# Performance work log

Hardware: AMD Instinct MI355X
Metric: run time of the kernel (lower is better)

The kernel has to match this reference:

```python
import jax, jax.numpy as jnp
import numpy as np


def _gcn_layer(x, W, b, src, dst, norm, n_nodes):
    # PyG GCNConv: h = x @ W, then degree-normalized scatter-add over edges (incl. self loops), then + bias
    h = x @ W                                   # [N, F_out]
    msg = h[src] * norm[:, None]                # [E+N, F_out]
    out = jax.ops.segment_sum(msg, dst, num_segments=n_nodes)
    return out + b


def _norm_and_loops(edge_index, n_nodes):
    # add self loops, compute symmetric normalization deg^-1/2[src]*deg^-1/2[dst]
    loop = jnp.arange(n_nodes, dtype=edge_index.dtype)
    src = jnp.concatenate([edge_index[0], loop])
    dst = jnp.concatenate([edge_index[1], loop])
    deg = jax.ops.segment_sum(jnp.ones_like(dst, dtype=jnp.float32), dst, num_segments=n_nodes)
    dinv = jnp.where(deg > 0, jax.lax.rsqrt(deg), 0.0)
    norm = dinv[src] * dinv[dst]
    return src, dst, norm


def setup_inputs() -> dict:
    key = jax.random.key(0)
    k1, k2, k3, k4 = jax.random.split(key, 4)
    N, E, F = 100000, 1600000, 512
    x = jax.random.normal(k1, (N, F), dtype=jnp.float32)
    edge_index = jax.random.randint(k2, (2, E), 0, N, dtype=jnp.int64)
    W1 = jax.random.normal(k3, (F, 128), dtype=jnp.float32) * (1.0 / np.sqrt(F))
    b1 = jnp.zeros((128,), dtype=jnp.float32)
    W2 = jax.random.normal(k4, (128, 64), dtype=jnp.float32) * (1.0 / np.sqrt(128))
    b2 = jnp.zeros((64,), dtype=jnp.float32)
    return {"x": x, "edge_index": edge_index, "W1": W1, "b1": b1, "W2": W2, "b2": b2}


def reference(x, edge_index, W1, b1, W2, b2):
    n_nodes = x.shape[0]
    src, dst, norm = _norm_and_loops(edge_index, n_nodes)
    h = jax.nn.relu(_gcn_layer(x, W1, b1, src, dst, norm, n_nodes))
    z = jax.nn.relu(_gcn_layer(h, W2, b2, src, dst, norm, n_nodes))
    return z
```

## Files before the change

### kernel.cpp

```cpp
#include <hip/hip_runtime.h>

#define SCAN_B 1024

using f16x8 = __attribute__((ext_vector_type(8))) _Float16;
using f32x4 = __attribute__((ext_vector_type(4))) float;
typedef _Float16 half4v __attribute__((ext_vector_type(4)));
typedef _Float16 half8v __attribute__((ext_vector_type(8)));


__global__ void init_kernel(int* __restrict__ cnt, int* __restrict__ fillc, int N,
                            const float* __restrict__ W1, _Float16* __restrict__ W1t, int K1, int N1,
                            const float* __restrict__ W2, _Float16* __restrict__ W2t, int K2, int N2) {
  int i = blockIdx.x * blockDim.x + threadIdx.x;
  if (i < N) { cnt[i] = 0; fillc[i] = 0; }
  const int n1 = K1 * N1;
  if (i < n1) {
    int k = i / N1, n = i % N1;
    W1t[(size_t)n * K1 + k] = (_Float16)W1[i];
  } else if (i < n1 + K2 * N2) {
    int j = i - n1;
    int k = j / N2, n = j % N2;
    W2t[(size_t)n * K2 + k] = (_Float16)W2[j];
  }
}

__global__ void count_kernel(const int* __restrict__ ei, int* __restrict__ cnt, int E) {
  int i = blockIdx.x * blockDim.x + threadIdx.x;
  if (i < E) atomicAdd(&cnt[ei[E + i]], 1);
}

__global__ void scan1_kernel(const int* __restrict__ cnt, int* __restrict__ rowstart,
                             int* __restrict__ bsum, float* __restrict__ dinv, int n) {
  __shared__ int sm[SCAN_B];
  const int t = threadIdx.x;
  const int i = blockIdx.x * SCAN_B + t;
  int c = (i < n) ? cnt[i] : 0;
  if (i < n) dinv[i] = rsqrtf((float)(c + 1));
  int v = (i < n) ? (c + 1) : 0;
  sm[t] = v;
  __syncthreads();
  for (int off = 1; off < SCAN_B; off <<= 1) {
    int x = (t >= off) ? sm[t - off] : 0;
    __syncthreads();
    if (t >= off) sm[t] += x;
    __syncthreads();
  }
  if (i < n) rowstart[i] = sm[t] - v;
  if (t == SCAN_B - 1) bsum[blockIdx.x] = sm[t];
}

__global__ void scan2_kernel(int* __restrict__ bsum, int nb) {
  __shared__ int sm[SCAN_B];
  const int t = threadIdx.x;
  int v = (t < nb) ? bsum[t] : 0;
  sm[t] = v;
  __syncthreads();
  for (int off = 1; off < SCAN_B; off <<= 1) {
    int x = (t >= off) ? sm[t - off] : 0;
    __syncthreads();
    if (t >= off) sm[t] += x;
    __syncthreads();
  }
  if (t < nb) bsum[t] = sm[t] - v;
}

__global__ void scan3_kernel(int* __restrict__ rowstart, const int* __restrict__ bsum, int n) {
  int i = blockIdx.x * blockDim.x + threadIdx.x;
  if (i < n) rowstart[i] += bsum[i / SCAN_B];
}

__global__ void fillself_kernel(const int* __restrict__ ei, int* __restrict__ fillc,
                                const int* __restrict__ rowstart, const int* __restrict__ cnt,
                                const float* __restrict__ dinv, float2* __restrict__ ew,
                                int E, int N) {
  int i = blockIdx.x * blockDim.x + threadIdx.x;
  if (i < E) {
    int s = ei[i];
    int d = ei[E + i];
    int p = atomicAdd(&fillc[d], 1);
    ew[rowstart[d] + p] = make_float2(__int_as_float(s), dinv[s] * dinv[d]);
  } else if (i < E + N) {
    int n = i - E;
    float dn = dinv[n];
    ew[rowstart[n] + cnt[n]] = make_float2(__int_as_float(n), dn * dn);
  }
}


template <int BM, int BN, typename AT, typename CT>
__global__ void __launch_bounds__(512, 2)
gemm_mfma_kernel(const AT* __restrict__ A, const _Float16* __restrict__ Wt,
                 CT* __restrict__ C, int M, int K) {
  constexpr int BK   = 32;
  constexpr int LDK  = 40;
  constexpr int MR   = BM / 2 / 16;
  constexpr int NR   = BN / 4 / 16;
  constexpr int N    = BN;
  constexpr int LDC  = NR * 16 + 4;
  constexpr int SMA  = (BM + BN) * LDK * 2;
  constexpr int SME  = 8 * 16 * LDC * 4;
  constexpr int SMEM = SMA > SME ? SMA : SME;

  __shared__ __align__(16) char smem[SMEM];
  _Float16* Asm = (_Float16*)smem;
  _Float16* Bsm = Asm + (size_t)BM * LDK;

  const int tid  = threadIdx.x;
  const int lane = tid & 63;
  const int w    = tid >> 6;
  const int wm   = w >> 2;
  const int wn   = w & 3;
  const int fr   = lane & 15;
  const int fq   = lane >> 4;
  const int m0   = blockIdx.x * BM;

  constexpr bool A32 = sizeof(AT) == 4;
  const int a_c = A32 ? (tid & 7) : (tid & 3);
  const int a_m = A32 ? (tid >> 3) : (tid >> 2);
  const int br  = tid >> 2;
  const int bj  = tid & 3;

  float4 av32[2];
  uint4  av16;
  uint4  bt;

  auto loadA = [&](int kt) {
    if constexpr (A32) {
#pragma unroll
      for (int p = 0; p < 2; ++p) {
        const int gm = m0 + a_m + 64 * p;
        av32[p] = (gm < M) ? *(const float4*)&A[(size_t)gm * K + kt + 4 * a_c]
                           : make_float4(0.f, 0.f, 0.f, 0.f);
      }
    } else {
      const int gm = m0 + a_m;
      av16 = (gm < M) ? *(const uint4*)&A[(size_t)gm * K + kt + 8 * a_c]
                      : make_uint4(0u, 0u, 0u, 0u);
    }
  };
  auto loadB = [&](int kt) {
    if (tid < BN * 4) bt = *(const uint4*)&Wt[(size_t)br * K + kt + 8 * bj];
  };

  f32x4 acc[MR][NR] = {};

  loadA(0);
  loadB(0);

  for (int kt = 0; kt < K; kt += BK) {
    __syncthreads();

    if constexpr (A32) {
#pragma unroll
      for (int p = 0; p < 2; ++p) {
        const int r = a_m + 64 * p;
        half4v hv = {(_Float16)av32[p].x, (_Float16)av32[p].y,
                     (_Float16)av32[p].z, (_Float16)av32[p].w};
        *(half4v*)((char*)Asm + r * (LDK * 2) + a_c * 8) = hv;
      }
    } else {
      *(uint4*)((char*)Asm + a_m * (LDK * 2) + a_c * 16) = av16;
    }
    if (tid < BN * 4) *(uint4*)((char*)Bsm + br * (LDK * 2) + 16 * bj) = bt;
    __syncthreads();

    if (kt + BK < K) {
      loadA(kt + BK);
      loadB(kt + BK);
    }

    f16x8 bfrag[NR];
#pragma unroll
    for (int ni = 0; ni < NR; ++ni) {
      const int r = wn * (NR * 16) + ni * 16 + fr;
      bfrag[ni] = *(const f16x8*)((const char*)Bsm + r * (LDK * 2) + fq * 16);
    }
#pragma unroll
    for (int mi = 0; mi < MR; ++mi) {
      const int r = wm * 64 + mi * 16 + fr;
      f16x8 afrag = *(const f16x8*)((const char*)Asm + r * (LDK * 2) + fq * 16);
#pragma unroll
      for (int ni = 0; ni < NR; ++ni)
        acc[mi][ni] = __builtin_amdgcn_mfma_f32_16x16x32_f16(afrag, bfrag[ni], acc[mi][ni], 0, 0, 0);
    }
  }

  __syncthreads();
  {
    float* cst = (float*)smem + (size_t)w * (16 * LDC);
    constexpr int CPR   = NR * 4;
    constexpr int EPASS = (16 * CPR + 63) / 64;
#pragma unroll
    for (int mi = 0; mi < MR; ++mi) {
#pragma unroll
      for (int ni = 0; ni < NR; ++ni)
#pragma unroll
        for (int r = 0; r < 4; ++r)
          cst[(fq * 4 + r) * LDC + ni * 16 + fr] = acc[mi][ni][r];
#pragma unroll
      for (int p = 0; p < EPASS; ++p) {
        const int idx = p * 64 + lane;
        if (idx < 16 * CPR) {
          const int row = idx / CPR;
          const int ch  = idx % CPR;
          const int gm  = m0 + wm * 64 + mi * 16 + row;
          float4 v = *(const float4*)&cst[row * LDC + ch * 4];
          if (gm < M) {
            if constexpr (sizeof(CT) == 2) {
              half4v hv = {(_Float16)v.x, (_Float16)v.y, (_Float16)v.z, (_Float16)v.w};
              *(half4v*)&C[(size_t)gm * N + wn * (NR * 16) + ch * 4] = hv;
            } else {
              *(float4*)&C[(size_t)gm * N + wn * (NR * 16) + ch * 4] = v;
            }
          }
        }
      }
    }
  }
}


template <int F, typename OT>
__global__ void agg_kernel(const _Float16* __restrict__ hin, const int* __restrict__ rowstart,
                           const int* __restrict__ cnt, const float2* __restrict__ ew,
                           const float* __restrict__ bias, OT* __restrict__ outp, int N) {
  constexpr int LPE = F / 8;
  constexpr int EPW = 64 / LPE;
  const int wave = (int)((blockIdx.x * (size_t)blockDim.x + threadIdx.x) >> 6);
  if (wave >= N) return;
  const int lane = threadIdx.x & 63;
  const int sub  = lane / LPE;
  const int c    = lane % LPE;
  const int n    = wave;

  const int beg = rowstart[n];
  const int end = beg + cnt[n] + 1;

  float acc[8] = {};
  int j = beg + sub;
  for (; j + 3 * EPW < end; j += 4 * EPW) {
    const float2 e0 = ew[j];
    const float2 e1 = ew[j + EPW];
    const float2 e2 = ew[j + 2 * EPW];
    const float2 e3 = ew[j + 3 * EPW];
    const half8v v0 = *(const half8v*)&hin[(size_t)__float_as_int(e0.x) * F + c * 8];
    const half8v v1 = *(const half8v*)&hin[(size_t)__float_as_int(e1.x) * F + c * 8];
    const half8v v2 = *(const half8v*)&hin[(size_t)__float_as_int(e2.x) * F + c * 8];
    const half8v v3 = *(const half8v*)&hin[(size_t)__float_as_int(e3.x) * F + c * 8];
#pragma unroll
    for (int i = 0; i < 8; ++i) {
      acc[i] = fmaf((float)v0[i], e0.y, acc[i]);
      acc[i] = fmaf((float)v1[i], e1.y, acc[i]);
      acc[i] = fmaf((float)v2[i], e2.y, acc[i]);
      acc[i] = fmaf((float)v3[i], e3.y, acc[i]);
    }
  }
  for (; j < end; j += EPW) {
    const float2 e = ew[j];
    const half8v v = *(const half8v*)&hin[(size_t)__float_as_int(e.x) * F + c * 8];
#pragma unroll
    for (int i = 0; i < 8; ++i) acc[i] = fmaf((float)v[i], e.y, acc[i]);
  }

#pragma unroll
  for (int d = LPE; d < 64; d <<= 1)
#pragma unroll
    for (int i = 0; i < 8; ++i) acc[i] += __shfl_xor(acc[i], d);

  if (lane < LPE) {
    const float4 b0 = *(const float4*)&bias[c * 8];
    const float4 b1 = *(const float4*)&bias[c * 8 + 4];
    float r[8];
    r[0] = fmaxf(acc[0] + b0.x, 0.f);
    r[1] = fmaxf(acc[1] + b0.y, 0.f);
    r[2] = fmaxf(acc[2] + b0.z, 0.f);
    r[3] = fmaxf(acc[3] + b0.w, 0.f);
    r[4] = fmaxf(acc[4] + b1.x, 0.f);
    r[5] = fmaxf(acc[5] + b1.y, 0.f);
    r[6] = fmaxf(acc[6] + b1.z, 0.f);
    r[7] = fmaxf(acc[7] + b1.w, 0.f);
    if constexpr (sizeof(OT) == 2) {
      half8v hv;
#pragma unroll
      for (int i = 0; i < 8; ++i) hv[i] = (_Float16)r[i];
      *(half8v*)&outp[(size_t)n * F + c * 8] = hv;
    } else {
      *(float4*)&outp[(size_t)n * F + c * 8]     = make_float4(r[0], r[1], r[2], r[3]);
      *(float4*)&outp[(size_t)n * F + c * 8 + 4] = make_float4(r[4], r[5], r[6], r[7]);
    }
  }
}


extern "C" void kernel_launch(void* const* d_in, const int* in_sizes, int n_in,
                              void* d_out, int out_size, void* d_ws, size_t ws_size,
                              hipStream_t stream) {
  const float* x  = (const float*)d_in[0];
  const int*   ei = (const int*)d_in[1];
  const float* W1 = (const float*)d_in[2];
  const float* b1 = (const float*)d_in[3];
  const float* W2 = (const float*)d_in[4];
  const float* b2 = (const float*)d_in[5];
  float* out = (float*)d_out;

  const int F1 = in_sizes[3];
  const int F2 = in_sizes[5];
  const int F0 = in_sizes[2] / F1;
  const int N  = in_sizes[0] / F0;
  const int E  = in_sizes[1] / 2;

  char* ws = (char*)d_ws;
  size_t off = 0;
  auto alloc = [&](size_t bytes) -> void* {
    void* p = ws + off;
    off = (off + bytes + 255) & ~(size_t)255;
    return p;
  };

  int*    cnt      = (int*)alloc((size_t)N * 4);
  int*    fillc    = (int*)alloc((size_t)N * 4);
  int*    rowstart = (int*)alloc((size_t)N * 4);
  float*  dinv     = (float*)alloc((size_t)N * 4);
  const int nb     = (N + SCAN_B - 1) / SCAN_B;
  int*    bsum     = (int*)alloc((size_t)nb * 4);
  float2* ew       = (float2*)alloc(((size_t)E + N) * 8);
  _Float16* h      = (_Float16*)alloc((size_t)N * F1 * 2);
  _Float16* h1     = (_Float16*)alloc((size_t)N * F1 * 2);
  _Float16* h2     = h;
  _Float16* W1t    = (_Float16*)alloc((size_t)F0 * F1 * 2);
  _Float16* W2t    = (_Float16*)alloc((size_t)F1 * F2 * 2);

  const int initElems = (N > F0 * F1 + F1 * F2) ? N : (F0 * F1 + F1 * F2);
  init_kernel<<<(initElems + 255) / 256, 256, 0, stream>>>(
      cnt, fillc, N, W1, W1t, F0, F1, W2, W2t, F1, F2);
  count_kernel<<<(E + 255) / 256, 256, 0, stream>>>(ei, cnt, E);
  scan1_kernel<<<nb, SCAN_B, 0, stream>>>(cnt, rowstart, bsum, dinv, N);
  scan2_kernel<<<1, SCAN_B, 0, stream>>>(bsum, nb);
  scan3_kernel<<<(N + 255) / 256, 256, 0, stream>>>(rowstart, bsum, N);
  fillself_kernel<<<(E + N + 255) / 256, 256, 0, stream>>>(ei, fillc, rowstart, cnt, dinv, ew, E, N);

  gemm_mfma_kernel<128, 128, float, _Float16><<<(N + 127) / 128, 512, 0, stream>>>(x, W1t, h, N, F0);
  {
    const long blocks = ((long)N * 64 + 255) / 256;
    agg_kernel<128, _Float16><<<(int)blocks, 256, 0, stream>>>(h, rowstart, cnt, ew, b1, h1, N);
  }

  gemm_mfma_kernel<128, 64, _Float16, _Float16><<<(N + 127) / 128, 512, 0, stream>>>(h1, W2t, h2, N, F1);
  {
    const long blocks = ((long)N * 64 + 255) / 256;
    agg_kernel<64, float><<<(int)blocks, 256, 0, stream>>>(h2, rowstart, cnt, ew, b2, out, N);
  }
}
```

Baseline: 345.1 us.

## Double-buffer GEMM LDS tiles and fold scan3 block offsets into consumers

The MFMA GEMM now uses two LDS buffers per operand. The next tile is stored into the alternate buffer after the current tile's MFMAs, which leaves one barrier per K-step instead of two. Separately, the scan3 kernel launch is removed; fillself and agg add the block prefix bsum[n>>10] on the fly when reading rowstart. This costs double the LDS footprint, which may lower occupancy, plus one extra small load per node or edge.

```diff
diff --git a/kernel.cpp b/kernel.cpp
--- a/kernel.cpp
+++ b/kernel.cpp
@@ -64,25 +64,20 @@
   if (t < nb) bsum[t] = sm[t] - v;
 }
 
-__global__ void scan3_kernel(int* __restrict__ rowstart, const int* __restrict__ bsum, int n) {
-  int i = blockIdx.x * blockDim.x + threadIdx.x;
-  if (i < n) rowstart[i] += bsum[i / SCAN_B];
-}
-
 __global__ void fillself_kernel(const int* __restrict__ ei, int* __restrict__ fillc,
-                                const int* __restrict__ rowstart, const int* __restrict__ cnt,
-                                const float* __restrict__ dinv, float2* __restrict__ ew,
-                                int E, int N) {
+                                const int* __restrict__ rowstart, const int* __restrict__ bsum,
+                                const int* __restrict__ cnt, const float* __restrict__ dinv,
+                                float2* __restrict__ ew, int E, int N) {
   int i = blockIdx.x * blockDim.x + threadIdx.x;
   if (i < E) {
     int s = ei[i];
     int d = ei[E + i];
     int p = atomicAdd(&fillc[d], 1);
-    ew[rowstart[d] + p] = make_float2(__int_as_float(s), dinv[s] * dinv[d]);
+    ew[rowstart[d] + bsum[d >> 10] + p] = make_float2(__int_as_float(s), dinv[s] * dinv[d]);
   } else if (i < E + N) {
     int n = i - E;
     float dn = dinv[n];
-    ew[rowstart[n] + cnt[n]] = make_float2(__int_as_float(n), dn * dn);
+    ew[rowstart[n] + bsum[n >> 10] + cnt[n]] = make_float2(__int_as_float(n), dn * dn);
   }
 }
 
@@ -97,13 +92,15 @@
   constexpr int NR   = BN / 4 / 16;
   constexpr int N    = BN;
   constexpr int LDC  = NR * 16 + 4;
-  constexpr int SMA  = (BM + BN) * LDK * 2;
+  constexpr int SMA  = 2 * (BM + BN) * LDK * 2;
   constexpr int SME  = 8 * 16 * LDC * 4;
   constexpr int SMEM = SMA > SME ? SMA : SME;
 
   __shared__ __align__(16) char smem[SMEM];
-  _Float16* Asm = (_Float16*)smem;
-  _Float16* Bsm = Asm + (size_t)BM * LDK;
+  _Float16* A0 = (_Float16*)smem;
+  _Float16* B0 = A0 + (size_t)BM * LDK;
+  _Float16* A1 = B0 + (size_t)BN * LDK;
+  _Float16* B1 = A1 + (size_t)BM * LDK;
 
   const int tid  = threadIdx.x;
   const int lane = tid & 63;
@@ -141,15 +138,7 @@
   auto loadB = [&](int kt) {
     if (tid < BN * 4) bt = *(const uint4*)&Wt[(size_t)br * K + kt + 8 * bj];
   };
-
-  f32x4 acc[MR][NR] = {};
-
-  loadA(0);
-  loadB(0);
-
-  for (int kt = 0; kt < K; kt += BK) {
-    __syncthreads();
-
+  auto storeAB = [&](_Float16* Asm, _Float16* Bsm) {
     if constexpr (A32) {
 #pragma unroll
       for (int p = 0; p < 2; ++p) {
@@ -162,9 +151,24 @@
       *(uint4*)((char*)Asm + a_m * (LDK * 2) + a_c * 16) = av16;
     }
     if (tid < BN * 4) *(uint4*)((char*)Bsm + br * (LDK * 2) + 16 * bj) = bt;
-    __syncthreads();
-
-    if (kt + BK < K) {
+  };
+
+  f32x4 acc[MR][NR] = {};
+
+  loadA(0);
+  loadB(0);
+  storeAB(A0, B0);
+  __syncthreads();
+
+  int buf = 0;
+  for (int kt = 0; kt < K; kt += BK, buf ^= 1) {
+    const _Float16* Ac = buf ? A1 : A0;
+    const _Float16* Bc = buf ? B1 : B0;
+    _Float16* An = buf ? A0 : A1;
+    _Float16* Bn = buf ? B0 : B1;
+    const bool more = (kt + BK < K);
+
+    if (more) {
       loadA(kt + BK);
       loadB(kt + BK);
     }
@@ -173,15 +177,20 @@
 #pragma unroll
     for (int ni = 0; ni < NR; ++ni) {
       const int r = wn * (NR * 16) + ni * 16 + fr;
-      bfrag[ni] = *(const f16x8*)((const char*)Bsm + r * (LDK * 2) + fq * 16);
+      bfrag[ni] = *(const f16x8*)((const char*)Bc + r * (LDK * 2) + fq * 16);
     }
 #pragma unroll
     for (int mi = 0; mi < MR; ++mi) {
       const int r = wm * 64 + mi * 16 + fr;
-      f16x8 afrag = *(const f16x8*)((const char*)Asm + r * (LDK * 2) + fq * 16);
+      f16x8 afrag = *(const f16x8*)((const char*)Ac + r * (LDK * 2) + fq * 16);
 #pragma unroll
       for (int ni = 0; ni < NR; ++ni)
         acc[mi][ni] = __builtin_amdgcn_mfma_f32_16x16x32_f16(afrag, bfrag[ni], acc[mi][ni], 0, 0, 0);
+    }
+
+    if (more) {
+      storeAB(An, Bn);
+      __syncthreads();
     }
   }
 
@@ -222,8 +231,9 @@
 
 template <int F, typename OT>
 __global__ void agg_kernel(const _Float16* __restrict__ hin, const int* __restrict__ rowstart,
-                           const int* __restrict__ cnt, const float2* __restrict__ ew,
-                           const float* __restrict__ bias, OT* __restrict__ outp, int N) {
+                           const int* __restrict__ bsum, const int* __restrict__ cnt,
+                           const float2* __restrict__ ew, const float* __restrict__ bias,
+                           OT* __restrict__ outp, int N) {
   constexpr int LPE = F / 8;
   constexpr int EPW = 64 / LPE;
   const int wave = (int)((blockIdx.x * (size_t)blockDim.x + threadIdx.x) >> 6);
@@ -233,7 +243,7 @@
   const int c    = lane % LPE;
   const int n    = wave;
 
-  const int beg = rowstart[n];
+  const int beg = rowstart[n] + bsum[n >> 10];
   const int end = beg + cnt[n] + 1;
 
   float acc[8] = {};
@@ -336,18 +346,17 @@
   count_kernel<<<(E + 255) / 256, 256, 0, stream>>>(ei, cnt, E);
   scan1_kernel<<<nb, SCAN_B, 0, stream>>>(cnt, rowstart, bsum, dinv, N);
   scan2_kernel<<<1, SCAN_B, 0, stream>>>(bsum, nb);
-  scan3_kernel<<<(N + 255) / 256, 256, 0, stream>>>(rowstart, bsum, N);
-  fillself_kernel<<<(E + N + 255) / 256, 256, 0, stream>>>(ei, fillc, rowstart, cnt, dinv, ew, E, N);
+  fillself_kernel<<<(E + N + 255) / 256, 256, 0, stream>>>(ei, fillc, rowstart, bsum, cnt, dinv, ew, E, N);
 
   gemm_mfma_kernel<128, 128, float, _Float16><<<(N + 127) / 128, 512, 0, stream>>>(x, W1t, h, N, F0);
   {
     const long blocks = ((long)N * 64 + 255) / 256;
-    agg_kernel<128, _Float16><<<(int)blocks, 256, 0, stream>>>(h, rowstart, cnt, ew, b1, h1, N);
+    agg_kernel<128, _Float16><<<(int)blocks, 256, 0, stream>>>(h, rowstart, bsum, cnt, ew, b1, h1, N);
   }
 
   gemm_mfma_kernel<128, 64, _Float16, _Float16><<<(N + 127) / 128, 512, 0, stream>>>(h1, W2t, h2, N, F1);
   {
     const long blocks = ((long)N * 64 + 255) / 256;
-    agg_kernel<64, float><<<(int)blocks, 256, 0, stream>>>(h2, rowstart, cnt, ew, b2, out, N);
-  }
-}
+    agg_kernel<64, float><<<(int)blocks, 256, 0, stream>>>(h2, rowstart, bsum, cnt, ew, b2, out, N);
+  }
+}
```

Measured after the change: 343.5 us. No clear change (-0.5%).
